# Optimization experiments

Measured on AMD Instinct MI355X. Metric: run time of the kernel, lower is better.

## Reference

```python
import jax, jax.numpy as jnp
import numpy as np

B, T, D = 4, 4096, 1024
P = 64  # d_model / n_head

def setup_inputs() -> dict:
    key = jax.random.key(0)
    k1, k2, k3 = jax.random.split(key, 3)
    x = jax.random.normal(k1, (B, T, D), dtype=jnp.float32)
    Wqkv = jax.random.normal(k2, (D, 3 * P), dtype=jnp.float32) * (1.0 / np.sqrt(D))
    bqkv = jax.random.normal(k3, (3 * P,), dtype=jnp.float32) * 0.01
    return {"x": x, "Wqkv": Wqkv, "bqkv": bqkv}

def reference(x, Wqkv, bqkv):
    Bv, Tv, Cv = x.shape
    qkv = (x @ Wqkv + bqkv).reshape(Bv, Tv, 3, P)  # [B,T,3,p]
    q, k, v = qkv[:, :, 0, :], qkv[:, :, 1, :], qkv[:, :, 2, :]
    # raw scores (source applies NO 1/sqrt(p) scaling)
    S = jnp.einsum('btp,bsp->bts', q, k)  # [B,T,T]
    causal = jnp.tril(jnp.ones((Tv, Tv), dtype=bool))
    S = jnp.where(causal[None, :, :], S, jnp.float32(-jnp.inf))
    Pm = jax.nn.softmax(S, axis=-1)
    O = jnp.einsum('bts,bsp->btp', Pm, v)  # [B,T,p]
    return O
```

## Files before the change

### kernel.cpp

```cpp
#include <hip/hip_runtime.h>
#include <hip/hip_fp16.h>

#define B_ 4
#define T_ 4096
#define D_ 1024

typedef _Float16 h8 __attribute__((ext_vector_type(8)));
typedef _Float16 h4 __attribute__((ext_vector_type(4)));
typedef float f32x4 __attribute__((ext_vector_type(4)));

#define LOG2E 1.44269504088896340736f
#define MASKV -3.0e38f
#define MINIT -1.0e30f
#define EXP2(x) __builtin_amdgcn_exp2f(x)

__global__ __launch_bounds__(256) void wt_kernel(const float* __restrict__ W,
                                                 _Float16* __restrict__ Wt) {
    __shared__ _Float16 Tr[192][20];
    const int tid = threadIdx.x, k0 = blockIdx.x * 16;
#pragma unroll
    for (int i = 0; i < 3; i++) {
        int fi = tid + 256 * i;
        int r = fi / 48, c4 = fi % 48;
        float4 v = *(const float4*)(W + (size_t)(k0 + r) * 192 + c4 * 4);
        Tr[c4 * 4 + 0][r] = (_Float16)v.x;
        Tr[c4 * 4 + 1][r] = (_Float16)v.y;
        Tr[c4 * 4 + 2][r] = (_Float16)v.z;
        Tr[c4 * 4 + 3][r] = (_Float16)v.w;
    }
    __syncthreads();
#pragma unroll
    for (int i = 0; i < 3; i++) {
        int oi = tid + 256 * i;
        int n = oi >> 2, kq = oi & 3;
        *(h4*)(Wt + (size_t)n * D_ + k0 + kq * 4) = *(const h4*)&Tr[n][kq * 4];
    }
}

__global__ __launch_bounds__(256, 2) void proj_kernel(
    const float* __restrict__ x, const _Float16* __restrict__ Wt,
    const float* __restrict__ bias,
    _Float16* __restrict__ qh, _Float16* __restrict__ kh, _Float16* __restrict__ vh)
{
    __shared__ __align__(16) char psm[60928];
    _Float16* Asp = (_Float16*)psm;
    _Float16* Bsp = (_Float16*)(psm + 8704);
    _Float16* Ostp = (_Float16*)psm;
    const int tid = threadIdx.x;
    const int w = tid >> 6, lane = tid & 63, quad = lane >> 4, l16 = lane & 15;
    const int row0 = blockIdx.x * 32;
    const int ng3 = w * 3;

    float bvals[3];
#pragma unroll
    for (int nt = 0; nt < 3; nt++) bvals[nt] = bias[(ng3 + nt) * 16 + l16];

    f32x4 acc[2][3];
#pragma unroll
    for (int u = 0; u < 2; u++)
#pragma unroll
        for (int i = 0; i < 3; i++) acc[u][i] = (f32x4){0.f, 0.f, 0.f, 0.f};

    const int arow = tid >> 3, ac = (tid & 7) * 4;
    const float* xrow = x + (size_t)(row0 + arow) * D_;

    float4 xa[4];
    h8 wreg[12];
#pragma unroll
    for (int p = 0; p < 4; p++) xa[p] = *(const float4*)(xrow + p * 32 + ac);
#pragma unroll
    for (int p = 0; p < 12; p++) {
        int f = tid + 256 * p; int n = f >> 4, c = (f & 15) * 8;
        wreg[p] = *(const h8*)(Wt + (size_t)n * D_ + c);
    }

    for (int it = 0; it < 8; it++) {
        if (it) __syncthreads();
#pragma unroll
        for (int p = 0; p < 4; p++) {
            h4 av;
            av[0] = (_Float16)xa[p].x; av[1] = (_Float16)xa[p].y;
            av[2] = (_Float16)xa[p].z; av[3] = (_Float16)xa[p].w;
            *(h4*)(Asp + arow * 136 + p * 32 + ac) = av;
        }
#pragma unroll
        for (int p = 0; p < 12; p++) {
            int f = tid + 256 * p; int n = f >> 4, c = (f & 15) * 8;
            *(h8*)(Bsp + n * 136 + c) = wreg[p];
        }
        __syncthreads();
        if (it + 1 < 8) {
            const int k0 = (it + 1) * 128;
#pragma unroll
            for (int p = 0; p < 4; p++) xa[p] = *(const float4*)(xrow + k0 + p * 32 + ac);
#pragma unroll
            for (int p = 0; p < 12; p++) {
                int f = tid + 256 * p; int n = f >> 4, c = (f & 15) * 8;
                wreg[p] = *(const h8*)(Wt + (size_t)n * D_ + k0 + c);
            }
        }
#pragma unroll
        for (int kk = 0; kk < 4; kk++) {
            h8 a0 = *(const h8*)(Asp + l16 * 136 + kk * 32 + quad * 8);
            h8 a1 = *(const h8*)(Asp + (16 + l16) * 136 + kk * 32 + quad * 8);
#pragma unroll
            for (int nt = 0; nt < 3; nt++) {
                h8 b0 = *(const h8*)(Bsp + ((ng3 + nt) * 16 + l16) * 136 + kk * 32 + quad * 8);
                acc[0][nt] = __builtin_amdgcn_mfma_f32_16x16x32_f16(a0, b0, acc[0][nt], 0, 0, 0);
                acc[1][nt] = __builtin_amdgcn_mfma_f32_16x16x32_f16(a1, b0, acc[1][nt], 0, 0, 0);
            }
        }
    }

    __syncthreads();
#pragma unroll
    for (int u = 0; u < 2; u++)
#pragma unroll
        for (int nt = 0; nt < 3; nt++) {
            int n = (ng3 + nt) * 16 + l16;
            float scale = (n < 64) ? LOG2E : 1.0f;
#pragma unroll
            for (int reg = 0; reg < 4; reg++)
                Ostp[(16 * u + quad * 4 + reg) * 200 + n] =
                    (_Float16)((acc[u][nt][reg] + bvals[nt]) * scale);
        }
    __syncthreads();
    {
        const int mrow = tid >> 3, c0 = (tid & 7) * 8;
        _Float16* dsts[3] = {qh, kh, vh};
#pragma unroll
        for (int g = 0; g < 3; g++)
            *(h8*)(dsts[g] + (size_t)(row0 + mrow) * 64 + c0) =
                *(const h8*)(Ostp + mrow * 200 + g * 64 + c0);
    }
}

__global__ __launch_bounds__(256, 3) void attn_kernel(
    const _Float16* __restrict__ qh, const _Float16* __restrict__ kh,
    const _Float16* __restrict__ vh, float* __restrict__ out,
    _Float16* __restrict__ Opart, float2* __restrict__ ml,
    int lgC, int NC1, int direct, int q8, int total)
{
    __shared__ _Float16 Ks[2][64][72];
    __shared__ _Float16 Vt[2][64][72];
    const int tid = threadIdx.x;
    const int w = tid >> 6, lane = tid & 63, quad = lane >> 4, l16 = lane & 15;
    const int C = 1 << lgC;

    const int bid = blockIdx.x;
    const int cid = (bid & 7) * q8 + (bid >> 3);
    if (cid >= total) return;

    const int b = cid / NC1;
    int rem = cid - b * NC1;
    int qt2 = 0, k0 = 0, cnt = 1;
    for (int i = 0; i < 32; i++) {
        int nc = (2 * i + 2 + C - 1) >> lgC;
        if (rem < nc) { qt2 = i; k0 = rem << lgC; cnt = min(C, 2 * i + 2 - k0); break; }
        rem -= nc;
    }
    const size_t base = (size_t)b * T_ * 64;
    const int qbase = qt2 * 128 + w * 32;

    h8 qf[2][2];
#pragma unroll
    for (int u = 0; u < 2; u++) {
        const _Float16* qp = qh + base + (size_t)(qbase + u * 16 + l16) * 64 + quad * 8;
        qf[u][0] = *(const h8*)qp;
        qf[u][1] = *(const h8*)(qp + 32);
    }

    f32x4 o[8];
#pragma unroll
    for (int i = 0; i < 8; i++) o[i] = (f32x4){0.f, 0.f, 0.f, 0.f};
    float m[2] = {MINIT, MINIT}, l[2] = {0.f, 0.f};

    const int krow = tid >> 3, kc0 = (tid & 7) * 8;
    const int vp0 = (tid & 15) * 4, vc0 = (tid >> 4) * 4;
    h8 kreg[2];
    h4 vreg[4];
    {
        const _Float16* kp = kh + base + (size_t)(k0 * 64) * 64;
        kreg[0] = *(const h8*)(kp + (size_t)krow * 64 + kc0);
        kreg[1] = *(const h8*)(kp + (size_t)(krow + 32) * 64 + kc0);
        const _Float16* vp = vh + base + (size_t)(k0 * 64 + vc0) * 64 + vp0;
#pragma unroll
        for (int i = 0; i < 4; i++) vreg[i] = *(const h4*)(vp + (size_t)i * 64);
    }

    const int kend = k0 + cnt;
    for (int kt = k0; kt < kend; kt++) {
        const int buf = kt & 1;
        *(h8*)&Ks[buf][krow][kc0] = kreg[0];
        *(h8*)&Ks[buf][krow + 32][kc0] = kreg[1];
#pragma unroll
        for (int j = 0; j < 4; j++) {
            h4 t;
            t[0] = vreg[0][j]; t[1] = vreg[1][j]; t[2] = vreg[2][j]; t[3] = vreg[3][j];
            *(h4*)&Vt[buf][vp0 + j][vc0] = t;
        }
        if (kt + 1 < kend) {
            const _Float16* kp = kh + base + (size_t)((kt + 1) * 64) * 64;
            kreg[0] = *(const h8*)(kp + (size_t)krow * 64 + kc0);
            kreg[1] = *(const h8*)(kp + (size_t)(krow + 32) * 64 + kc0);
            const _Float16* vp = vh + base + (size_t)((kt + 1) * 64 + vc0) * 64 + vp0;
#pragma unroll
            for (int i = 0; i < 4; i++) vreg[i] = *(const h4*)(vp + (size_t)i * 64);
        }
        __syncthreads();

        const bool skip = (kt * 64) > (qbase + 31);
        if (!skip) {
            f32x4 s[2][4];
            __builtin_amdgcn_s_setprio(1);
#pragma unroll
            for (int nt = 0; nt < 4; nt++) {
                h8 kf0 = *(const h8*)&Ks[buf][nt * 16 + l16][quad * 8];
                h8 kf1 = *(const h8*)&Ks[buf][nt * 16 + l16][32 + quad * 8];
#pragma unroll
                for (int u = 0; u < 2; u++) {
                    f32x4 c = (f32x4){0.f, 0.f, 0.f, 0.f};
                    c = __builtin_amdgcn_mfma_f32_16x16x32_f16(kf0, qf[u][0], c, 0, 0, 0);
                    c = __builtin_amdgcn_mfma_f32_16x16x32_f16(kf1, qf[u][1], c, 0, 0, 0);
                    s[u][nt] = c;
                }
            }
            __builtin_amdgcn_s_setprio(0);

            h4 pf[2][4];
#pragma unroll
            for (int u = 0; u < 2; u++) {
                const int qrow = qbase + u * 16 + l16;
                if (kt * 64 + 63 > qbase + u * 16) {
#pragma unroll
                    for (int nt = 0; nt < 4; nt++)
#pragma unroll
                        for (int reg = 0; reg < 4; reg++) {
                            int sg = kt * 64 + nt * 16 + quad * 4 + reg;
                            if (sg > qrow) s[u][nt][reg] = MASKV;
                        }
                }
                float mx = s[u][0][0];
#pragma unroll
                for (int nt = 0; nt < 4; nt++)
#pragma unroll
                    for (int reg = 0; reg < 4; reg++) mx = fmaxf(mx, s[u][nt][reg]);
                mx = fmaxf(mx, __shfl_xor(mx, 16));
                mx = fmaxf(mx, __shfl_xor(mx, 32));
                if (!__all(mx <= m[u] + 8.0f)) {
                    float mnew = fmaxf(m[u], mx);
                    float alpha = EXP2(m[u] - mnew);
                    m[u] = mnew;
                    l[u] *= alpha;
#pragma unroll
                    for (int pt = 0; pt < 4; pt++)
#pragma unroll
                        for (int reg = 0; reg < 4; reg++) o[u * 4 + pt][reg] *= alpha;
                }
                float rs = 0.f;
#pragma unroll
                for (int nt = 0; nt < 4; nt++) {
                    h4 ph;
#pragma unroll
                    for (int reg = 0; reg < 4; reg++) {
                        float p = EXP2(s[u][nt][reg] - m[u]);
                        rs += p;
                        ph[reg] = (_Float16)p;
                    }
                    pf[u][nt] = ph;
                }
                rs += __shfl_xor(rs, 16);
                rs += __shfl_xor(rs, 32);
                l[u] += rs;
            }

            __builtin_amdgcn_s_setprio(1);
#pragma unroll
            for (int pt = 0; pt < 4; pt++)
#pragma unroll
                for (int nt = 0; nt < 4; nt++) {
                    h4 vf = *(const h4*)&Vt[buf][pt * 16 + l16][nt * 16 + quad * 4];
                    o[pt]     = __builtin_amdgcn_mfma_f32_16x16x16f16(vf, pf[0][nt], o[pt], 0, 0, 0);
                    o[4 + pt] = __builtin_amdgcn_mfma_f32_16x16x16f16(vf, pf[1][nt], o[4 + pt], 0, 0, 0);
                }
            __builtin_amdgcn_s_setprio(0);
        }
    }

    if (direct) {
#pragma unroll
        for (int u = 0; u < 2; u++) {
            float linv = 1.0f / l[u];
            int trow = qt2 * 128 + w * 32 + u * 16 + l16;
#pragma unroll
            for (int pt = 0; pt < 4; pt++)
#pragma unroll
                for (int reg = 0; reg < 4; reg++)
                    out[base + (size_t)trow * 64 + pt * 16 + quad * 4 + reg] =
                        o[u * 4 + pt][reg] * linv;
        }
    } else {
        __syncthreads();
        _Float16* St = &Ks[0][0][0];
#pragma unroll
        for (int u = 0; u < 2; u++) {
            int r = w * 32 + u * 16 + l16;
#pragma unroll
            for (int pt = 0; pt < 4; pt++) {
                h4 ph;
#pragma unroll
                for (int reg = 0; reg < 4; reg++) ph[reg] = (_Float16)o[u * 4 + pt][reg];
                *(h4*)&St[r * 72 + pt * 16 + quad * 4] = ph;
            }
            if (quad == 0) ml[(size_t)cid * 128 + r] = make_float2(m[u], l[u]);
        }
        __syncthreads();
        _Float16* op = Opart + (size_t)cid * 8192;
        const int r = tid >> 1, c0 = (tid & 1) * 32;
#pragma unroll
        for (int j = 0; j < 4; j++)
            *(h8*)(op + r * 64 + c0 + 8 * j) = *(const h8*)&St[r * 72 + c0 + 8 * j];
    }
}

__global__ __launch_bounds__(256) void combine_kernel(
    const _Float16* __restrict__ Opart, const float2* __restrict__ ml,
    float* __restrict__ out, int lgC, int NC1)
{
    const int C = 1 << lgC;
    const int task = blockIdx.x;
    const int b = task >> 8, tile = (task >> 3) & 31, rg = task & 7;
    int pref = 0;
    for (int i = 0; i < tile; i++) pref += (2 * i + 2 + C - 1) >> lgC;
    const int cbase = b * NC1 + pref;
    const int nch = (2 * tile + 2 + C - 1) >> lgC;

    const int r = rg * 16 + (threadIdx.x >> 4);
    const int c0 = (threadIdx.x & 15) * 4;

    float M = MINIT;
    for (int i = 0; i < nch; i++) M = fmaxf(M, ml[(size_t)(cbase + i) * 128 + r].x);
    float L = 0.f, acc[4] = {0.f, 0.f, 0.f, 0.f};
    for (int i = 0; i < nch; i++) {
        float2 v = ml[(size_t)(cbase + i) * 128 + r];
        float sc = EXP2(v.x - M);
        L += sc * v.y;
        h4 x4 = *(const h4*)(Opart + (size_t)(cbase + i) * 8192 + (size_t)r * 64 + c0);
#pragma unroll
        for (int t = 0; t < 4; t++) acc[t] += sc * (float)x4[t];
    }
    float inv = 1.0f / L;
    float4 res = { acc[0]*inv, acc[1]*inv, acc[2]*inv, acc[3]*inv };
    *(float4*)(out + ((size_t)b * T_ + tile * 128 + r) * 64 + c0) = res;
}

extern "C" void kernel_launch(void* const* d_in, const int* in_sizes, int n_in,
                              void* d_out, int out_size, void* d_ws, size_t ws_size,
                              hipStream_t stream) {
    const float* x    = (const float*)d_in[0];
    const float* W    = (const float*)d_in[1];
    const float* bias = (const float*)d_in[2];
    float* out = (float*)d_out;
    char* ws = (char*)d_ws;
    _Float16* qh = (_Float16*)(ws);
    _Float16* kh = (_Float16*)(ws + (size_t)2 * 1024 * 1024);
    _Float16* vh = (_Float16*)(ws + (size_t)4 * 1024 * 1024);
    _Float16* Wt = (_Float16*)(ws + (size_t)6 * 1024 * 1024);
    const size_t pbase = (size_t)8 * 1024 * 1024;

    int lgC = -1, nc1 = 32;
    for (int lg = 3; lg <= 6; lg++) {
        int C = 1 << lg, n1 = 0;
        for (int i = 0; i < 32; i++) n1 += (2 * i + 2 + C - 1) >> lg;
        size_t need = pbase + (size_t)4 * n1 * (8192 * 2 + 128 * 8);
        if (need <= ws_size) { lgC = lg; nc1 = n1; break; }
    }
    int direct = (lgC < 0) ? 1 : 0;
    if (direct) { lgC = 6; nc1 = 32; }
    _Float16* Opart = (_Float16*)(ws + pbase);
    float2*   mlp   = (float2*)(ws + pbase + (size_t)4 * nc1 * 8192 * 2);

    const int total = 4 * nc1;
    const int q8 = (total + 7) / 8;

    wt_kernel<<<64, 256, 0, stream>>>(W, Wt);
    proj_kernel<<<512, 256, 0, stream>>>(x, Wt, bias, qh, kh, vh);
    attn_kernel<<<8 * q8, 256, 0, stream>>>(qh, kh, vh, out, Opart, mlp,
                                            lgC, nc1, direct, q8, total);
    if (!direct)
        combine_kernel<<<1024, 256, 0, stream>>>(Opart, mlp, out, lgC, nc1);
}
```

Before: 143.8 us.

## Read projection weights directly from global and double-buffer activation tile in LDS

The QKV projection kernel no longer stages the fp16 weight tile through shared memory. Each wave loads its MFMA B operands straight from global memory, which is expected to hit L2 because every block reads the same weights. The activation tile is double-buffered in LDS, so each k-step needs one barrier instead of two. LDS use drops from about 60KB to 17KB, which should allow higher occupancy. The trade-off is that weight loads now sit directly in front of the MFMAs with no register prefetch, which risks exposing global-memory latency.

```diff
diff --git a/kernel.cpp b/kernel.cpp
--- a/kernel.cpp
+++ b/kernel.cpp
@@ -42,9 +42,8 @@
     const float* __restrict__ bias,
     _Float16* __restrict__ qh, _Float16* __restrict__ kh, _Float16* __restrict__ vh)
 {
-    __shared__ __align__(16) char psm[60928];
+    __shared__ __align__(16) char psm[17408];
     _Float16* Asp = (_Float16*)psm;
-    _Float16* Bsp = (_Float16*)(psm + 8704);
     _Float16* Ostp = (_Float16*)psm;
     const int tid = threadIdx.x;
     const int w = tid >> 6, lane = tid & 63, quad = lane >> 4, l16 = lane & 15;
@@ -64,55 +63,57 @@
     const int arow = tid >> 3, ac = (tid & 7) * 4;
     const float* xrow = x + (size_t)(row0 + arow) * D_;
 
+    const _Float16* wp[3];
+#pragma unroll
+    for (int nt = 0; nt < 3; nt++)
+        wp[nt] = Wt + (size_t)((ng3 + nt) * 16 + l16) * D_ + quad * 8;
+
     float4 xa[4];
-    h8 wreg[12];
 #pragma unroll
     for (int p = 0; p < 4; p++) xa[p] = *(const float4*)(xrow + p * 32 + ac);
 #pragma unroll
-    for (int p = 0; p < 12; p++) {
-        int f = tid + 256 * p; int n = f >> 4, c = (f & 15) * 8;
-        wreg[p] = *(const h8*)(Wt + (size_t)n * D_ + c);
-    }
+    for (int p = 0; p < 4; p++) {
+        h4 av;
+        av[0] = (_Float16)xa[p].x; av[1] = (_Float16)xa[p].y;
+        av[2] = (_Float16)xa[p].z; av[3] = (_Float16)xa[p].w;
+        *(h4*)(Asp + arow * 136 + p * 32 + ac) = av;
+    }
+#pragma unroll
+    for (int p = 0; p < 4; p++) xa[p] = *(const float4*)(xrow + 128 + p * 32 + ac);
+    __syncthreads();
 
     for (int it = 0; it < 8; it++) {
-        if (it) __syncthreads();
-#pragma unroll
-        for (int p = 0; p < 4; p++) {
-            h4 av;
-            av[0] = (_Float16)xa[p].x; av[1] = (_Float16)xa[p].y;
-            av[2] = (_Float16)xa[p].z; av[3] = (_Float16)xa[p].w;
-            *(h4*)(Asp + arow * 136 + p * 32 + ac) = av;
-        }
-#pragma unroll
-        for (int p = 0; p < 12; p++) {
-            int f = tid + 256 * p; int n = f >> 4, c = (f & 15) * 8;
-            *(h8*)(Bsp + n * 136 + c) = wreg[p];
-        }
-        __syncthreads();
+        const int cur = it & 1;
         if (it + 1 < 8) {
-            const int k0 = (it + 1) * 128;
-#pragma unroll
-            for (int p = 0; p < 4; p++) xa[p] = *(const float4*)(xrow + k0 + p * 32 + ac);
-#pragma unroll
-            for (int p = 0; p < 12; p++) {
-                int f = tid + 256 * p; int n = f >> 4, c = (f & 15) * 8;
-                wreg[p] = *(const h8*)(Wt + (size_t)n * D_ + k0 + c);
-            }
-        }
+#pragma unroll
+            for (int p = 0; p < 4; p++) {
+                h4 av;
+                av[0] = (_Float16)xa[p].x; av[1] = (_Float16)xa[p].y;
+                av[2] = (_Float16)xa[p].z; av[3] = (_Float16)xa[p].w;
+                *(h4*)(Asp + (cur ^ 1) * 4352 + arow * 136 + p * 32 + ac) = av;
+            }
+            if (it + 2 < 8) {
+                const int k0 = (it + 2) * 128;
+#pragma unroll
+                for (int p = 0; p < 4; p++)
+                    xa[p] = *(const float4*)(xrow + k0 + p * 32 + ac);
+            }
+        }
+        const int kbase = it * 128;
 #pragma unroll
         for (int kk = 0; kk < 4; kk++) {
-            h8 a0 = *(const h8*)(Asp + l16 * 136 + kk * 32 + quad * 8);
-            h8 a1 = *(const h8*)(Asp + (16 + l16) * 136 + kk * 32 + quad * 8);
+            h8 a0 = *(const h8*)(Asp + cur * 4352 + l16 * 136 + kk * 32 + quad * 8);
+            h8 a1 = *(const h8*)(Asp + cur * 4352 + (16 + l16) * 136 + kk * 32 + quad * 8);
 #pragma unroll
             for (int nt = 0; nt < 3; nt++) {
-                h8 b0 = *(const h8*)(Bsp + ((ng3 + nt) * 16 + l16) * 136 + kk * 32 + quad * 8);
+                h8 b0 = *(const h8*)(wp[nt] + kbase + kk * 32);
                 acc[0][nt] = __builtin_amdgcn_mfma_f32_16x16x32_f16(a0, b0, acc[0][nt], 0, 0, 0);
                 acc[1][nt] = __builtin_amdgcn_mfma_f32_16x16x32_f16(a1, b0, acc[1][nt], 0, 0, 0);
             }
         }
-    }
-
-    __syncthreads();
+        __syncthreads();
+    }
+
 #pragma unroll
     for (int u = 0; u < 2; u++)
 #pragma unroll
```

Result: slower. 153.9 us (+7.0%).

## Double attention query tile to 256 rows for more K/V reuse per block

Applied to the files above, without the earlier changes.

Each attention block now handles 256 query rows instead of 128, so each wave owns 64 rows. Every K/V tile staged in shared memory then feeds twice as many MFMAs, which cuts global and LDS traffic per unit of work. The chunk schedule, partial-output layout, workspace sizing and combine kernel are all rewritten to match the larger tile. The cost is higher register pressure, with occupancy lowered from 3 to 2 blocks per CU. The grid also shrinks to about half as many, larger blocks, which adds masked work on the causal diagonal and can hurt load balance across CUs.

```diff
diff --git a/kernel.cpp b/kernel.cpp
--- a/kernel.cpp
+++ b/kernel.cpp
@@ -135,14 +135,13 @@
     }
 }
 
-__global__ __launch_bounds__(256, 3) void attn_kernel(
+__global__ __launch_bounds__(256, 2) void attn_kernel(
     const _Float16* __restrict__ qh, const _Float16* __restrict__ kh,
     const _Float16* __restrict__ vh, float* __restrict__ out,
     _Float16* __restrict__ Opart, float2* __restrict__ ml,
     int lgC, int NC1, int direct, int q8, int total)
 {
-    __shared__ _Float16 Ks[2][64][72];
-    __shared__ _Float16 Vt[2][64][72];
+    __shared__ _Float16 SM[4][64][72];
     const int tid = threadIdx.x;
     const int w = tid >> 6, lane = tid & 63, quad = lane >> 4, l16 = lane & 15;
     const int C = 1 << lgC;
@@ -153,27 +152,28 @@
 
     const int b = cid / NC1;
     int rem = cid - b * NC1;
-    int qt2 = 0, k0 = 0, cnt = 1;
-    for (int i = 0; i < 32; i++) {
-        int nc = (2 * i + 2 + C - 1) >> lgC;
-        if (rem < nc) { qt2 = i; k0 = rem << lgC; cnt = min(C, 2 * i + 2 - k0); break; }
+    int qt = 0, k0 = 0, cnt = 1;
+    for (int i = 0; i < 16; i++) {
+        int nk = 4 * i + 4;
+        int nc = (nk + C - 1) >> lgC;
+        if (rem < nc) { qt = i; k0 = rem << lgC; cnt = min(C, nk - k0); break; }
         rem -= nc;
     }
     const size_t base = (size_t)b * T_ * 64;
-    const int qbase = qt2 * 128 + w * 32;
-
-    h8 qf[2][2];
-#pragma unroll
-    for (int u = 0; u < 2; u++) {
+    const int qbase = qt * 256 + w * 64;
+
+    h8 qf[4][2];
+#pragma unroll
+    for (int u = 0; u < 4; u++) {
         const _Float16* qp = qh + base + (size_t)(qbase + u * 16 + l16) * 64 + quad * 8;
         qf[u][0] = *(const h8*)qp;
         qf[u][1] = *(const h8*)(qp + 32);
     }
 
-    f32x4 o[8];
-#pragma unroll
-    for (int i = 0; i < 8; i++) o[i] = (f32x4){0.f, 0.f, 0.f, 0.f};
-    float m[2] = {MINIT, MINIT}, l[2] = {0.f, 0.f};
+    f32x4 o[16];
+#pragma unroll
+    for (int i = 0; i < 16; i++) o[i] = (f32x4){0.f, 0.f, 0.f, 0.f};
+    float m[4] = {MINIT, MINIT, MINIT, MINIT}, l[4] = {0.f, 0.f, 0.f, 0.f};
 
     const int krow = tid >> 3, kc0 = (tid & 7) * 8;
     const int vp0 = (tid & 15) * 4, vc0 = (tid >> 4) * 4;
@@ -191,13 +191,13 @@
     const int kend = k0 + cnt;
     for (int kt = k0; kt < kend; kt++) {
         const int buf = kt & 1;
-        *(h8*)&Ks[buf][krow][kc0] = kreg[0];
-        *(h8*)&Ks[buf][krow + 32][kc0] = kreg[1];
+        *(h8*)&SM[buf][krow][kc0] = kreg[0];
+        *(h8*)&SM[buf][krow + 32][kc0] = kreg[1];
 #pragma unroll
         for (int j = 0; j < 4; j++) {
             h4 t;
             t[0] = vreg[0][j]; t[1] = vreg[1][j]; t[2] = vreg[2][j]; t[3] = vreg[3][j];
-            *(h4*)&Vt[buf][vp0 + j][vc0] = t;
+            *(h4*)&SM[2 + buf][vp0 + j][vc0] = t;
         }
         if (kt + 1 < kend) {
             const _Float16* kp = kh + base + (size_t)((kt + 1) * 64) * 64;
@@ -209,16 +209,16 @@
         }
         __syncthreads();
 
-        const bool skip = (kt * 64) > (qbase + 31);
+        const bool skip = (kt * 64) > (qbase + 63);
         if (!skip) {
-            f32x4 s[2][4];
+            f32x4 s[4][4];
             __builtin_amdgcn_s_setprio(1);
 #pragma unroll
             for (int nt = 0; nt < 4; nt++) {
-                h8 kf0 = *(const h8*)&Ks[buf][nt * 16 + l16][quad * 8];
-                h8 kf1 = *(const h8*)&Ks[buf][nt * 16 + l16][32 + quad * 8];
-#pragma unroll
-                for (int u = 0; u < 2; u++) {
+                h8 kf0 = *(const h8*)&SM[buf][nt * 16 + l16][quad * 8];
+                h8 kf1 = *(const h8*)&SM[buf][nt * 16 + l16][32 + quad * 8];
+#pragma unroll
+                for (int u = 0; u < 4; u++) {
                     f32x4 c = (f32x4){0.f, 0.f, 0.f, 0.f};
                     c = __builtin_amdgcn_mfma_f32_16x16x32_f16(kf0, qf[u][0], c, 0, 0, 0);
                     c = __builtin_amdgcn_mfma_f32_16x16x32_f16(kf1, qf[u][1], c, 0, 0, 0);
@@ -227,9 +227,9 @@
             }
             __builtin_amdgcn_s_setprio(0);
 
-            h4 pf[2][4];
-#pragma unroll
-            for (int u = 0; u < 2; u++) {
+            h4 pf[4][4];
+#pragma unroll
+            for (int u = 0; u < 4; u++) {
                 const int qrow = qbase + u * 16 + l16;
                 if (kt * 64 + 63 > qbase + u * 16) {
 #pragma unroll
@@ -279,9 +279,11 @@
             for (int pt = 0; pt < 4; pt++)
 #pragma unroll
                 for (int nt = 0; nt < 4; nt++) {
-                    h4 vf = *(const h4*)&Vt[buf][pt * 16 + l16][nt * 16 + quad * 4];
-                    o[pt]     = __builtin_amdgcn_mfma_f32_16x16x16f16(vf, pf[0][nt], o[pt], 0, 0, 0);
-                    o[4 + pt] = __builtin_amdgcn_mfma_f32_16x16x16f16(vf, pf[1][nt], o[4 + pt], 0, 0, 0);
+                    h4 vf = *(const h4*)&SM[2 + buf][pt * 16 + l16][nt * 16 + quad * 4];
+#pragma unroll
+                    for (int u = 0; u < 4; u++)
+                        o[u * 4 + pt] = __builtin_amdgcn_mfma_f32_16x16x16f16(
+                            vf, pf[u][nt], o[u * 4 + pt], 0, 0, 0);
                 }
             __builtin_amdgcn_s_setprio(0);
         }
@@ -289,9 +291,9 @@
 
     if (direct) {
 #pragma unroll
-        for (int u = 0; u < 2; u++) {
+        for (int u = 0; u < 4; u++) {
             float linv = 1.0f / l[u];
-            int trow = qt2 * 128 + w * 32 + u * 16 + l16;
+            int trow = qt * 256 + w * 64 + u * 16 + l16;
 #pragma unroll
             for (int pt = 0; pt < 4; pt++)
 #pragma unroll
@@ -301,10 +303,10 @@
         }
     } else {
         __syncthreads();
-        _Float16* St = &Ks[0][0][0];
-#pragma unroll
-        for (int u = 0; u < 2; u++) {
-            int r = w * 32 + u * 16 + l16;
+        _Float16* St = &SM[0][0][0];
+#pragma unroll
+        for (int u = 0; u < 4; u++) {
+            int r = w * 64 + u * 16 + l16;
 #pragma unroll
             for (int pt = 0; pt < 4; pt++) {
                 h4 ph;
@@ -312,14 +314,14 @@
                 for (int reg = 0; reg < 4; reg++) ph[reg] = (_Float16)o[u * 4 + pt][reg];
                 *(h4*)&St[r * 72 + pt * 16 + quad * 4] = ph;
             }
-            if (quad == 0) ml[(size_t)cid * 128 + r] = make_float2(m[u], l[u]);
+            if (quad == 0) ml[(size_t)cid * 256 + r] = make_float2(m[u], l[u]);
         }
         __syncthreads();
-        _Float16* op = Opart + (size_t)cid * 8192;
-        const int r = tid >> 1, c0 = (tid & 1) * 32;
-#pragma unroll
-        for (int j = 0; j < 4; j++)
-            *(h8*)(op + r * 64 + c0 + 8 * j) = *(const h8*)&St[r * 72 + c0 + 8 * j];
+        _Float16* op = Opart + (size_t)cid * 16384;
+        const int r = tid;
+#pragma unroll
+        for (int j = 0; j < 8; j++)
+            *(h8*)(op + r * 64 + 8 * j) = *(const h8*)&St[r * 72 + 8 * j];
     }
 }
 
@@ -329,29 +331,29 @@
 {
     const int C = 1 << lgC;
     const int task = blockIdx.x;
-    const int b = task >> 8, tile = (task >> 3) & 31, rg = task & 7;
+    const int b = task >> 8, tile = (task >> 4) & 15, rg = task & 15;
     int pref = 0;
-    for (int i = 0; i < tile; i++) pref += (2 * i + 2 + C - 1) >> lgC;
+    for (int i = 0; i < tile; i++) pref += (4 * i + 4 + C - 1) >> lgC;
     const int cbase = b * NC1 + pref;
-    const int nch = (2 * tile + 2 + C - 1) >> lgC;
+    const int nch = (4 * tile + 4 + C - 1) >> lgC;
 
     const int r = rg * 16 + (threadIdx.x >> 4);
     const int c0 = (threadIdx.x & 15) * 4;
 
     float M = MINIT;
-    for (int i = 0; i < nch; i++) M = fmaxf(M, ml[(size_t)(cbase + i) * 128 + r].x);
+    for (int i = 0; i < nch; i++) M = fmaxf(M, ml[(size_t)(cbase + i) * 256 + r].x);
     float L = 0.f, acc[4] = {0.f, 0.f, 0.f, 0.f};
     for (int i = 0; i < nch; i++) {
-        float2 v = ml[(size_t)(cbase + i) * 128 + r];
+        float2 v = ml[(size_t)(cbase + i) * 256 + r];
         float sc = EXP2(v.x - M);
         L += sc * v.y;
-        h4 x4 = *(const h4*)(Opart + (size_t)(cbase + i) * 8192 + (size_t)r * 64 + c0);
+        h4 x4 = *(const h4*)(Opart + (size_t)(cbase + i) * 16384 + (size_t)r * 64 + c0);
 #pragma unroll
         for (int t = 0; t < 4; t++) acc[t] += sc * (float)x4[t];
     }
     float inv = 1.0f / L;
     float4 res = { acc[0]*inv, acc[1]*inv, acc[2]*inv, acc[3]*inv };
-    *(float4*)(out + ((size_t)b * T_ + tile * 128 + r) * 64 + c0) = res;
+    *(float4*)(out + ((size_t)b * T_ + tile * 256 + r) * 64 + c0) = res;
 }
 
 extern "C" void kernel_launch(void* const* d_in, const int* in_sizes, int n_in,
@@ -368,17 +370,17 @@
     _Float16* Wt = (_Float16*)(ws + (size_t)6 * 1024 * 1024);
     const size_t pbase = (size_t)8 * 1024 * 1024;
 
-    int lgC = -1, nc1 = 32;
+    int lgC = -1, nc1 = 16;
     for (int lg = 3; lg <= 6; lg++) {
         int C = 1 << lg, n1 = 0;
-        for (int i = 0; i < 32; i++) n1 += (2 * i + 2 + C - 1) >> lg;
-        size_t need = pbase + (size_t)4 * n1 * (8192 * 2 + 128 * 8);
+        for (int i = 0; i < 16; i++) n1 += (4 * i + 4 + C - 1) >> lg;
+        size_t need = pbase + (size_t)4 * n1 * (16384 * 2 + 256 * 8);
         if (need <= ws_size) { lgC = lg; nc1 = n1; break; }
     }
     int direct = (lgC < 0) ? 1 : 0;
-    if (direct) { lgC = 6; nc1 = 32; }
+    if (direct) { lgC = 6; nc1 = 16; }
     _Float16* Opart = (_Float16*)(ws + pbase);
-    float2*   mlp   = (float2*)(ws + pbase + (size_t)4 * nc1 * 8192 * 2);
+    float2*   mlp   = (float2*)(ws + pbase + (size_t)4 * nc1 * 16384 * 2);
 
     const int total = 4 * nc1;
     const int q8 = (total + 7) / 8;
```

Measured after the change: 147.8 us. 2.7% more time.
